# Kernel tuning notes

Measured on AMD Instinct MI355X. Metric: run time of the kernel, lower is better.

The kernel has to match this reference:

```python
import jax, jax.numpy as jnp
import numpy as np

B, S, IN, OUT, GS = 4, 2048, 4096, 4096, 256
NG = IN // GS  # number of groups per output channel


def setup_inputs() -> dict:
    key = jax.random.key(0)
    k1, k2, k3, k4 = jax.random.split(key, 4)
    x = jax.random.normal(k1, (B, S, IN), dtype=jnp.float32)
    # int4 codes stored in int8: values in [-8, 7]
    weight_int8 = jax.random.randint(k2, (OUT, IN), -8, 8, dtype=jnp.int32).astype(jnp.int8)
    scales = jax.random.uniform(k3, (OUT, NG), dtype=jnp.float32, minval=0.001, maxval=0.02)
    # zero points stored in scales_precision (float), integer-valued in int4 range
    zeros = jax.random.randint(k4, (OUT, NG), -8, 8, dtype=jnp.int32).astype(jnp.float32)
    return {"x": x, "weight_int8": weight_int8, "scales": scales, "zeros": zeros,
            "group_size": GS}


def per_token_dynamic_quant(x):
    """Asymmetric per-token int8 quantize -> dequantize (torchao decomposed ops)."""
    qmin, qmax = -128.0, 127.0
    mn = jnp.minimum(jnp.min(x, axis=-1, keepdims=True), 0.0)
    mx = jnp.maximum(jnp.max(x, axis=-1, keepdims=True), 0.0)
    eps = jnp.finfo(jnp.float32).eps
    scale = jnp.maximum((mx - mn) / (qmax - qmin), eps)
    # choose zero point minimizing error at whichever end is larger
    zp = jnp.where((qmin + mn / scale) + (qmax + mx / scale) > 0,
                   qmin - mn / scale, qmax - mx / scale)
    zp = jnp.clip(jnp.round(zp), qmin, qmax)
    q = jnp.clip(jnp.round(x / scale) + zp, qmin, qmax)
    return (q - zp) * scale


def dequant_per_channel_group(w_int8, scales, zeros, group_size):
    O, I = w_int8.shape
    g = I // group_size
    w = w_int8.reshape(O, g, group_size).astype(jnp.float32)
    w_dq = (w - zeros[:, :, None]) * scales[:, :, None]
    return w_dq.reshape(O, I)


def reference(x, weight_int8, scales, zeros, group_size):
    xq = per_token_dynamic_quant(x.astype(jnp.float32))
    w_dq = dequant_per_channel_group(weight_int8, scales, zeros, group_size)
    # F.linear: x @ w_dq.T  -> [B, S, OUT]
    return jnp.einsum('bsi,oi->bso', xq, w_dq)
```

## Files before the change

### kernel.cpp

```cpp
#include <hip/hip_runtime.h>
#include <hip/hip_bf16.h>
#include <stdint.h>

#define T_   8192
#define IN_  4096
#define OUT_ 4096
#define GS_  256
#define NG_  16

#define BM 128
#define BN 256
#define BK 128
#define KT (IN_ / BK)
#define GX (OUT_ / BN)
#define GY (T_ / BM)
#define NWG (GX * GY)

typedef int   v4i __attribute__((ext_vector_type(4)));
typedef float f4  __attribute__((ext_vector_type(4)));

__device__ __forceinline__ void gload16(const void* g, void* l) {
  __builtin_amdgcn_global_load_lds(
      (const __attribute__((address_space(1))) void*)g,
      (__attribute__((address_space(3))) void*)l, 16, 0, 0);
}

__global__ __launch_bounds__(256) void quant_kernel(
    const float* __restrict__ x, int8_t* __restrict__ q,
    float* __restrict__ tscale, float* __restrict__ tzp) {
  const int t = blockIdx.x;
  const int tid = threadIdx.x;
  const float* xr = x + (size_t)t * IN_ + tid * 16;
  float vals[16];
  {
    f4 v0 = *(const f4*)(xr);
    f4 v1 = *(const f4*)(xr + 4);
    f4 v2 = *(const f4*)(xr + 8);
    f4 v3 = *(const f4*)(xr + 12);
#pragma unroll
    for (int i = 0; i < 4; ++i) {
      vals[i] = v0[i]; vals[4 + i] = v1[i]; vals[8 + i] = v2[i]; vals[12 + i] = v3[i];
    }
  }
  float mn = 0.f, mx = 0.f;
#pragma unroll
  for (int i = 0; i < 16; ++i) { mn = fminf(mn, vals[i]); mx = fmaxf(mx, vals[i]); }
#pragma unroll
  for (int off = 32; off > 0; off >>= 1) {
    mn = fminf(mn, __shfl_xor(mn, off));
    mx = fmaxf(mx, __shfl_xor(mx, off));
  }
  __shared__ float smn[4], smx[4];
  if ((tid & 63) == 0) { smn[tid >> 6] = mn; smx[tid >> 6] = mx; }
  __syncthreads();
  mn = fminf(fminf(smn[0], smn[1]), fminf(smn[2], smn[3]));
  mx = fmaxf(fmaxf(smx[0], smx[1]), fmaxf(smx[2], smx[3]));

  const float eps = 1.1920928955078125e-7f;
  float scale = fmaxf((mx - mn) / 255.0f, eps);
  float rmn = mn / scale;
  float rmx = mx / scale;
  float zp0 = ((-128.0f + rmn) + (127.0f + rmx) > 0.0f) ? (-128.0f - rmn)
                                                        : (127.0f - rmx);
  float zp = fminf(fmaxf(rintf(zp0), -128.0f), 127.0f);
  if (tid == 0) { tscale[t] = scale; tzp[t] = zp; }

  const float inv = 1.0f / scale;
  v4i packed;
#pragma unroll
  for (int w = 0; w < 4; ++w) {
    int word = 0;
#pragma unroll
    for (int e = 0; e < 4; ++e) {
      float qf = rintf(vals[w * 4 + e] * inv) + zp;
      qf = fminf(fmaxf(qf, -128.0f), 127.0f);
      int qi = (int)qf;
      word |= (qi & 0xff) << (8 * e);
    }
    packed[w] = word;
  }
  *(v4i*)(q + (size_t)t * IN_ + tid * 16) = packed;
}

__global__ __launch_bounds__(256) void wprep_kernel(
    const int* __restrict__ w, const float* __restrict__ scales,
    const float* __restrict__ zeros, int8_t* __restrict__ wq,
    float* __restrict__ c1) {
  const int o = blockIdx.x;
  const int tid = threadIdx.x;
  const int g = tid >> 4;
  const int* wr = w + (size_t)o * IN_ + tid * 16;
  const int zi = (int)zeros[o * NG_ + g];
  int ssum = 0;
  v4i packed;
#pragma unroll
  for (int blk = 0; blk < 4; ++blk) {
    v4i ww = *(const v4i*)(wr + blk * 4);
    int word = 0;
#pragma unroll
    for (int e = 0; e < 4; ++e) {
      int wp = ww[e] - zi;
      ssum += wp;
      word |= (wp & 0xff) << (8 * e);
    }
    packed[blk] = word;
  }
  *(v4i*)(wq + (size_t)o * IN_ + tid * 16) = packed;
  ssum += __shfl_xor(ssum, 1);
  ssum += __shfl_xor(ssum, 2);
  ssum += __shfl_xor(ssum, 4);
  ssum += __shfl_xor(ssum, 8);
  __shared__ float part[NG_];
  if ((tid & 15) == 0) part[g] = scales[o * NG_ + g] * (float)ssum;
  __syncthreads();
  if (tid == 0) {
    float s = 0.f;
#pragma unroll
    for (int i = 0; i < NG_; ++i) s += part[i];
    c1[o] = s;
  }
}

__global__ __launch_bounds__(512, 2) void gemm_kernel(
    const int8_t* __restrict__ q, const int8_t* __restrict__ wq,
    const float* __restrict__ scales, const float* __restrict__ tscale,
    const float* __restrict__ tzp, const float* __restrict__ c1,
    float* __restrict__ out) {
  __shared__ int8_t As[2][BM * BK];
  __shared__ int8_t Bs[2][BN * BK];
  __shared__ float sSc[NG_ * BN];

  const int tid = threadIdx.x;
  const int lane = tid & 63;
  const int wid = tid >> 6;

  const int orig = blockIdx.y * GX + blockIdx.x;
  const int swz = (orig & 7) * (NWG / 8) + (orig >> 3);
  const int R0 = (swz >> 4) * BM;
  const int C0 = (swz & 15) * BN;

#pragma unroll
  for (int e = 0; e < 8; ++e) {
    int idx = tid + e * 512;
    int oc = idx >> 4, g = idx & 15;
    sSc[g * BN + oc] = scales[(size_t)(C0 + oc) * NG_ + g];
  }

  const int rA = tid >> 3;
  const int csw = ((tid & 7) ^ (rA & 7)) * 16;
  const int8_t* gA = q + (size_t)(R0 + rA) * IN_ + csw;
  const int8_t* gB = wq + (size_t)(C0 + rA) * IN_ + csw;

  const int wm = (wid >> 2) * 64;
  const int wn = (wid & 3) * 64;
  const int lm = lane & 15;
  const int quad = lane >> 4;
  const int o0 = (quad ^ (lm & 7)) * 16;
  const int aRow = (wm + lm) * BK;
  const int bRow = (wn + lm) * BK;

  v4i acci[4][4];
  float accf[4][4][4];
#pragma unroll
  for (int i = 0; i < 4; ++i)
#pragma unroll
    for (int j = 0; j < 4; ++j) {
      acci[i][j] = (v4i){0, 0, 0, 0};
#pragma unroll
      for (int r = 0; r < 4; ++r) accf[i][j][r] = 0.f;
    }

#pragma unroll
  for (int i = 0; i < 2; ++i)
    gload16(gA + (size_t)(i * 64) * IN_, &As[0][i * 8192 + tid * 16]);
#pragma unroll
  for (int i = 0; i < 4; ++i)
    gload16(gB + (size_t)(i * 64) * IN_, &Bs[0][i * 8192 + tid * 16]);
  __syncthreads();

  int cur = 0;
  for (int kt = 0; kt < KT; ++kt) {
    v4i af[4], bf[4];
    {
      const int co = o0;
#pragma unroll
      for (int i = 0; i < 4; ++i)
        af[i] = *(const v4i*)&As[cur][aRow + i * (16 * BK) + co];
#pragma unroll
      for (int j = 0; j < 4; ++j)
        bf[j] = *(const v4i*)&Bs[cur][bRow + j * (16 * BK) + co];
    }
    if (kt + 1 < KT) {
      const size_t koff = (size_t)(kt + 1) * BK;
#pragma unroll
      for (int i = 0; i < 2; ++i)
        gload16(gA + koff + (size_t)(i * 64) * IN_,
                &As[cur ^ 1][i * 8192 + tid * 16]);
#pragma unroll
      for (int i = 0; i < 4; ++i)
        gload16(gB + koff + (size_t)(i * 64) * IN_,
                &Bs[cur ^ 1][i * 8192 + tid * 16]);
    }
    __builtin_amdgcn_s_barrier();
    __builtin_amdgcn_s_setprio(1);
#pragma unroll
    for (int i = 0; i < 4; ++i)
#pragma unroll
      for (int j = 0; j < 4; ++j)
        acci[i][j] =
            __builtin_amdgcn_mfma_i32_16x16x64_i8(af[i], bf[j], acci[i][j], 0, 0, 0);
    __builtin_amdgcn_s_setprio(0);
    __builtin_amdgcn_s_barrier();

    {
      const int co = o0 ^ 64;
#pragma unroll
      for (int i = 0; i < 4; ++i)
        af[i] = *(const v4i*)&As[cur][aRow + i * (16 * BK) + co];
#pragma unroll
      for (int j = 0; j < 4; ++j)
        bf[j] = *(const v4i*)&Bs[cur][bRow + j * (16 * BK) + co];
    }
    __builtin_amdgcn_s_barrier();
    __builtin_amdgcn_s_setprio(1);
#pragma unroll
    for (int i = 0; i < 4; ++i)
#pragma unroll
      for (int j = 0; j < 4; ++j)
        acci[i][j] =
            __builtin_amdgcn_mfma_i32_16x16x64_i8(af[i], bf[j], acci[i][j], 0, 0, 0);
    __builtin_amdgcn_s_setprio(0);

    if (kt & 1) {
      const int g = kt >> 1;
      float sj[4];
#pragma unroll
      for (int j = 0; j < 4; ++j) sj[j] = sSc[g * BN + wn + j * 16 + lm];
#pragma unroll
      for (int i = 0; i < 4; ++i)
#pragma unroll
        for (int j = 0; j < 4; ++j) {
#pragma unroll
          for (int r = 0; r < 4; ++r)
            accf[i][j][r] += sj[j] * (float)acci[i][j][r];
          acci[i][j] = (v4i){0, 0, 0, 0};
        }
    }
    __syncthreads();
    cur ^= 1;
  }

  float cj[4];
#pragma unroll
  for (int j = 0; j < 4; ++j) cj[j] = c1[C0 + wn + j * 16 + lm];
#pragma unroll
  for (int i = 0; i < 4; ++i) {
#pragma unroll
    for (int r = 0; r < 4; ++r) {
      const int row = R0 + wm + i * 16 + quad * 4 + r;
      const float tsc = tscale[row];
      const float tz = tzp[row];
#pragma unroll
      for (int j = 0; j < 4; ++j) {
        const int col = C0 + wn + j * 16 + lm;
        out[(size_t)row * OUT_ + col] = tsc * (accf[i][j][r] - tz * cj[j]);
      }
    }
  }
}

extern "C" void kernel_launch(void* const* d_in, const int* in_sizes, int n_in,
                              void* d_out, int out_size, void* d_ws, size_t ws_size,
                              hipStream_t stream) {
  const float* x = (const float*)d_in[0];
  const int* w = (const int*)d_in[1];
  const float* scales = (const float*)d_in[2];
  const float* zeros = (const float*)d_in[3];

  uint8_t* ws = (uint8_t*)d_ws;
  int8_t* q = (int8_t*)ws;
  int8_t* wq = (int8_t*)(ws + 33554432);
  float* tscale = (float*)(ws + 33554432 + 16777216);
  float* tzp = (float*)(ws + 33554432 + 16777216 + 32768);
  float* c1 = (float*)(ws + 33554432 + 16777216 + 65536);
  float* out = (float*)d_out;

  hipLaunchKernelGGL(quant_kernel, dim3(T_), dim3(256), 0, stream, x, q, tscale, tzp);
  hipLaunchKernelGGL(wprep_kernel, dim3(OUT_), dim3(256), 0, stream, w, scales, zeros, wq, c1);
  hipLaunchKernelGGL(gemm_kernel, dim3(GX, GY), dim3(512), 0, stream,
                     q, wq, scales, tscale, tzp, c1, out);
}
```

Measured before the change: 473.5 us.

## Double M tile to 256 and fold group scales into fp32 accumulation per MFMA

```diff
diff --git a/kernel.cpp b/kernel.cpp
--- a/kernel.cpp
+++ b/kernel.cpp
@@ -8,13 +8,12 @@
 #define GS_  256
 #define NG_  16
 
-#define BM 128
+#define BM 256
 #define BN 256
 #define BK 128
 #define KT (IN_ / BK)
 #define GX (OUT_ / BN)
 #define GY (T_ / BM)
-#define NWG (GX * GY)
 
 typedef int   v4i __attribute__((ext_vector_type(4)));
 typedef float f4  __attribute__((ext_vector_type(4)));
@@ -134,10 +133,8 @@
   const int lane = tid & 63;
   const int wid = tid >> 6;
 
-  const int orig = blockIdx.y * GX + blockIdx.x;
-  const int swz = (orig & 7) * (NWG / 8) + (orig >> 3);
-  const int R0 = (swz >> 4) * BM;
-  const int C0 = (swz & 15) * BN;
+  const int R0 = blockIdx.y * BM;
+  const int C0 = blockIdx.x * BN;
 
 #pragma unroll
   for (int e = 0; e < 8; ++e) {
@@ -151,27 +148,24 @@
   const int8_t* gA = q + (size_t)(R0 + rA) * IN_ + csw;
   const int8_t* gB = wq + (size_t)(C0 + rA) * IN_ + csw;
 
-  const int wm = (wid >> 2) * 64;
+  const int wm = (wid >> 2) * 128;
   const int wn = (wid & 3) * 64;
   const int lm = lane & 15;
   const int quad = lane >> 4;
   const int o0 = (quad ^ (lm & 7)) * 16;
-  const int aRow = (wm + lm) * BK;
-  const int bRow = (wn + lm) * BK;
-
-  v4i acci[4][4];
-  float accf[4][4][4];
+
+  float accf[8][4][4];
+#pragma unroll
+  for (int i = 0; i < 8; ++i)
+#pragma unroll
+    for (int j = 0; j < 4; ++j)
+#pragma unroll
+      for (int r = 0; r < 4; ++r) accf[i][j][r] = 0.f;
+
+  const v4i zero4 = (v4i){0, 0, 0, 0};
+
 #pragma unroll
   for (int i = 0; i < 4; ++i)
-#pragma unroll
-    for (int j = 0; j < 4; ++j) {
-      acci[i][j] = (v4i){0, 0, 0, 0};
-#pragma unroll
-      for (int r = 0; r < 4; ++r) accf[i][j][r] = 0.f;
-    }
-
-#pragma unroll
-  for (int i = 0; i < 2; ++i)
     gload16(gA + (size_t)(i * 64) * IN_, &As[0][i * 8192 + tid * 16]);
 #pragma unroll
   for (int i = 0; i < 4; ++i)
@@ -179,23 +173,47 @@
   __syncthreads();
 
   int cur = 0;
+  float sj[4];
   for (int kt = 0; kt < KT; ++kt) {
-    v4i af[4], bf[4];
-    {
-      const int co = o0;
+    if ((kt & 1) == 0) {
+      const int g = kt >> 1;
+#pragma unroll
+      for (int j = 0; j < 4; ++j) sj[j] = sSc[g * BN + wn + j * 16 + lm];
+    }
+    const int8_t* A = As[cur];
+    const int8_t* Bb = Bs[cur];
+    const size_t koff = (size_t)(kt + 1) * BK;
+    v4i af[4], bf[4], t0;
+
+#pragma unroll
+    for (int j = 0; j < 4; ++j)
+      bf[j] = *(const v4i*)&Bb[(wn + j * 16 + lm) * BK + o0];
+#pragma unroll
+    for (int i = 0; i < 4; ++i)
+      af[i] = *(const v4i*)&A[(wm + i * 16 + lm) * BK + o0];
+    if (kt + 1 < KT) {
 #pragma unroll
       for (int i = 0; i < 4; ++i)
-        af[i] = *(const v4i*)&As[cur][aRow + i * (16 * BK) + co];
-#pragma unroll
-      for (int j = 0; j < 4; ++j)
-        bf[j] = *(const v4i*)&Bs[cur][bRow + j * (16 * BK) + co];
-    }
-    if (kt + 1 < KT) {
-      const size_t koff = (size_t)(kt + 1) * BK;
-#pragma unroll
-      for (int i = 0; i < 2; ++i)
         gload16(gA + koff + (size_t)(i * 64) * IN_,
                 &As[cur ^ 1][i * 8192 + tid * 16]);
+    }
+    __builtin_amdgcn_s_barrier();
+    __builtin_amdgcn_s_setprio(1);
+#pragma unroll
+    for (int i = 0; i < 4; ++i)
+#pragma unroll
+      for (int j = 0; j < 4; ++j) {
+        t0 = __builtin_amdgcn_mfma_i32_16x16x64_i8(af[i], bf[j], zero4, 0, 0, 0);
+#pragma unroll
+        for (int r = 0; r < 4; ++r) accf[i][j][r] += sj[j] * (float)t0[r];
+      }
+    __builtin_amdgcn_s_setprio(0);
+    __builtin_amdgcn_s_barrier();
+
+#pragma unroll
+    for (int i = 0; i < 4; ++i)
+      af[i] = *(const v4i*)&A[(wm + 64 + i * 16 + lm) * BK + o0];
+    if (kt + 1 < KT) {
 #pragma unroll
       for (int i = 0; i < 4; ++i)
         gload16(gB + koff + (size_t)(i * 64) * IN_,
@@ -206,46 +224,49 @@
 #pragma unroll
     for (int i = 0; i < 4; ++i)
 #pragma unroll
-      for (int j = 0; j < 4; ++j)
-        acci[i][j] =
-            __builtin_amdgcn_mfma_i32_16x16x64_i8(af[i], bf[j], acci[i][j], 0, 0, 0);
+      for (int j = 0; j < 4; ++j) {
+        t0 = __builtin_amdgcn_mfma_i32_16x16x64_i8(af[i], bf[j], zero4, 0, 0, 0);
+#pragma unroll
+        for (int r = 0; r < 4; ++r) accf[4 + i][j][r] += sj[j] * (float)t0[r];
+      }
     __builtin_amdgcn_s_setprio(0);
     __builtin_amdgcn_s_barrier();
 
-    {
-      const int co = o0 ^ 64;
-#pragma unroll
-      for (int i = 0; i < 4; ++i)
-        af[i] = *(const v4i*)&As[cur][aRow + i * (16 * BK) + co];
-#pragma unroll
-      for (int j = 0; j < 4; ++j)
-        bf[j] = *(const v4i*)&Bs[cur][bRow + j * (16 * BK) + co];
-    }
+    const int o1 = o0 ^ 64;
+#pragma unroll
+    for (int j = 0; j < 4; ++j)
+      bf[j] = *(const v4i*)&Bb[(wn + j * 16 + lm) * BK + o1];
+#pragma unroll
+    for (int i = 0; i < 4; ++i)
+      af[i] = *(const v4i*)&A[(wm + i * 16 + lm) * BK + o1];
     __builtin_amdgcn_s_barrier();
     __builtin_amdgcn_s_setprio(1);
 #pragma unroll
     for (int i = 0; i < 4; ++i)
 #pragma unroll
-      for (int j = 0; j < 4; ++j)
-        acci[i][j] =
-            __builtin_amdgcn_mfma_i32_16x16x64_i8(af[i], bf[j], acci[i][j], 0, 0, 0);
+      for (int j = 0; j < 4; ++j) {
+        t0 = __builtin_amdgcn_mfma_i32_16x16x64_i8(af[i], bf[j], zero4, 0, 0, 0);
+#pragma unroll
+        for (int r = 0; r < 4; ++r) accf[i][j][r] += sj[j] * (float)t0[r];
+      }
     __builtin_amdgcn_s_setprio(0);
-
-    if (kt & 1) {
-      const int g = kt >> 1;
-      float sj[4];
-#pragma unroll
-      for (int j = 0; j < 4; ++j) sj[j] = sSc[g * BN + wn + j * 16 + lm];
-#pragma unroll
-      for (int i = 0; i < 4; ++i)
-#pragma unroll
-        for (int j = 0; j < 4; ++j) {
-#pragma unroll
-          for (int r = 0; r < 4; ++r)
-            accf[i][j][r] += sj[j] * (float)acci[i][j][r];
-          acci[i][j] = (v4i){0, 0, 0, 0};
-        }
-    }
+    __builtin_amdgcn_s_barrier();
+
+#pragma unroll
+    for (int i = 0; i < 4; ++i)
+      af[i] = *(const v4i*)&A[(wm + 64 + i * 16 + lm) * BK + o1];
+    __builtin_amdgcn_s_barrier();
+    __builtin_amdgcn_s_setprio(1);
+#pragma unroll
+    for (int i = 0; i < 4; ++i)
+#pragma unroll
+      for (int j = 0; j < 4; ++j) {
+        t0 = __builtin_amdgcn_mfma_i32_16x16x64_i8(af[i], bf[j], zero4, 0, 0, 0);
+#pragma unroll
+        for (int r = 0; r < 4; ++r) accf[4 + i][j][r] += sj[j] * (float)t0[r];
+      }
+    __builtin_amdgcn_s_setprio(0);
+
     __syncthreads();
     cur ^= 1;
   }
@@ -254,7 +275,7 @@
 #pragma unroll
   for (int j = 0; j < 4; ++j) cj[j] = c1[C0 + wn + j * 16 + lm];
 #pragma unroll
-  for (int i = 0; i < 4; ++i) {
+  for (int i = 0; i < 8; ++i) {
 #pragma unroll
     for (int r = 0; r < 4; ++r) {
       const int row = R0 + wm + i * 16 + quad * 4 + r;
```

Result: slower. 572.4 us (+20.9%).
